# Performance work log

Hardware: AMD Instinct MI355X
Metric: run time of the kernel (lower is better)

The kernel has to match this reference:

```python
import jax, jax.numpy as jnp
import numpy as np

N_NODES = 50000
N_EDGES = 640000
D_IN = 128
D_HID = 128
D_OUT = 128
N_GRAPHS = 64


def gcn_conv(x, edge_index, W, b, n_nodes):
    """PyG GCNConv: D^{-1/2} (A + I) D^{-1/2} X W + b (unit edge weights)."""
    src, dst = edge_index[0], edge_index[1]
    h = x @ W  # [N, d_out]
    # degree counts target-side edges plus the self loop
    deg = jax.ops.segment_sum(jnp.ones_like(dst, dtype=h.dtype), dst,
                              num_segments=n_nodes) + 1.0
    dinv = jax.lax.rsqrt(deg)  # deg >= 1 so always finite
    norm = dinv[src] * dinv[dst]  # [E]
    msg = h[src] * norm[:, None]  # gather + scale  [E, d_out]
    agg = jax.ops.segment_sum(msg, dst, num_segments=n_nodes)
    # self-loop contribution: norm_ii = dinv_i^2
    agg = agg + h * (dinv * dinv)[:, None]
    return agg + b


def global_mean_pool(x, batch, n_graphs):
    sums = jax.ops.segment_sum(x, batch, num_segments=n_graphs)
    cnt = jax.ops.segment_sum(jnp.ones((x.shape[0],), dtype=x.dtype), batch,
                              num_segments=n_graphs)
    return sums / jnp.maximum(cnt, 1.0)[:, None]


def setup_inputs() -> dict:
    key = jax.random.key(0)
    k = jax.random.split(key, 8)
    x = jax.random.normal(k[0], (N_NODES, D_IN), dtype=jnp.float32)
    edge_index = jax.random.randint(k[1], (2, N_EDGES), 0, N_NODES, dtype=jnp.int64)
    batch = jnp.sort(jax.random.randint(k[2], (N_NODES,), 0, N_GRAPHS, dtype=jnp.int64))
    s1 = 1.0 / np.sqrt(D_IN)
    s2 = 1.0 / np.sqrt(D_HID)
    W1 = jax.random.uniform(k[3], (D_IN, D_HID), jnp.float32, -s1, s1)
    b1 = jnp.zeros((D_HID,), jnp.float32)
    W2 = jax.random.uniform(k[4], (D_HID, D_OUT), jnp.float32, -s2, s2)
    b2 = jnp.zeros((D_OUT,), jnp.float32)
    return {"x": x, "edge_index": edge_index, "batch": batch,
            "W1": W1, "b1": b1, "W2": W2, "b2": b2}


def reference(x, edge_index, batch, W1, b1, W2, b2):
    n = x.shape[0]
    h = jax.nn.relu(gcn_conv(x, edge_index, W1, b1, n))
    h = gcn_conv(h, edge_index, W2, b2, n)
    return global_mean_pool(h, batch, N_GRAPHS)
```

## Files before the change

kernel.cpp:

```cpp
#include <hip/hip_runtime.h>


#define D 128
#define NGRAPH 64
#define SCAN_B 1024
#define AGG_BLOCKS 2048

typedef _Float16 h16x2 __attribute__((ext_vector_type(2)));
typedef _Float16 f16x8 __attribute__((ext_vector_type(8)));
typedef float    f32x4 __attribute__((ext_vector_type(4)));

__device__ __forceinline__ float2 h2f(unsigned u) {
    h16x2 h = __builtin_bit_cast(h16x2, u);
    return make_float2((float)h.x, (float)h.y);
}
__device__ __forceinline__ unsigned f2h(float x, float y) {
    h16x2 h;
    h.x = (_Float16)x;
    h.y = (_Float16)y;
    return __builtin_bit_cast(unsigned, h);
}

__global__ void zero_out_kernel(float* __restrict__ out, int n) {
    int i = blockIdx.x * blockDim.x + threadIdx.x;
    if (i < n) out[i] = 0.f;
}

__global__ __launch_bounds__(256) void conv_count_kernel(const float* __restrict__ X,
                                                         _Float16* __restrict__ Xh,
                                                         const float* __restrict__ W1,
                                                         _Float16* __restrict__ WB,
                                                         const int* __restrict__ ei,
                                                         int* __restrict__ deg,
                                                         int N, int E, int cb) {
    int b = (int)blockIdx.x;
    if (b < cb) {
        int idx = b * 256 + (int)threadIdx.x;
        int total = N * (D / 4);
        if (idx < total) {
            float4 v = ((const float4*)X)[idx];
            uint2 o;
            o.x = f2h(v.x, v.y);
            o.y = f2h(v.z, v.w);
            ((uint2*)Xh)[idx] = o;
        }
        return;
    }
    if (b < cb + 8) {
        int idx = (b - cb) * 256 + (int)threadIdx.x;
        int lane = idx & 63;
        int nt   = (idx >> 6) & 7;
        int kt   = idx >> 9;
        int col  = nt * 16 + (lane & 15);
        int krow = kt * 32 + (lane >> 4) * 8;
#pragma unroll
        for (int j = 0; j < 8; ++j)
            WB[idx * 8 + j] = (_Float16)W1[(krow + j) * D + col];
        return;
    }
    int e = (b - cb - 8) * 256 + (int)threadIdx.x;
    if (e < E) {
        int d = ei[E + e];
        if (d >= 0 && d < N) atomicAdd(&deg[d], 1);
    }
}

__global__ __launch_bounds__(SCAN_B) void block_scan_kernel(const int* __restrict__ deg,
                                                            int* __restrict__ rowstart,
                                                            int* __restrict__ bsum,
                                                            float* __restrict__ dinv,
                                                            int N) {
    __shared__ int sc[SCAN_B];
    int t = threadIdx.x;
    int i = blockIdx.x * SCAN_B + t;
    int orig = (i < N) ? deg[i] : 0;
    int v = orig;
    sc[t] = v;
    __syncthreads();
    for (int off = 1; off < SCAN_B; off <<= 1) {
        int add = (t >= off) ? sc[t - off] : 0;
        __syncthreads();
        v += add;
        sc[t] = v;
        __syncthreads();
    }
    if (i < N) {
        rowstart[i] = v - orig;
        dinv[i]     = rsqrtf((float)orig + 1.0f);
    }
    if (t == SCAN_B - 1) bsum[blockIdx.x] = v;
}

__global__ __launch_bounds__(SCAN_B) void finalize_scan_kernel(const int* __restrict__ bsum,
                                                               int* __restrict__ rowstart,
                                                               int* __restrict__ cursor,
                                                               int N, int nblk, int E) {
    __shared__ int s_off;
    if (threadIdx.x < 64) {
        int lane = (int)threadIdx.x;
        int v = (lane < nblk && lane < (int)blockIdx.x) ? bsum[lane] : 0;
        for (int off = 32; off > 0; off >>= 1) v += __shfl_down(v, off);
        if (lane == 0) s_off = v;
    }
    __syncthreads();
    int i = blockIdx.x * SCAN_B + threadIdx.x;
    if (i < N) {
        int rs = rowstart[i] + s_off;
        rowstart[i] = rs;
        cursor[i]   = rs;
    }
    if (blockIdx.x == 0 && threadIdx.x == 0) rowstart[N] = E;
}

__global__ __launch_bounds__(256) void gemm_fill_kernel(const _Float16* __restrict__ Xh,
                                                        const _Float16* __restrict__ WB,
                                                        const float* __restrict__ dinv,
                                                        _Float16* __restrict__ Gh,
                                                        const int* __restrict__ ei,
                                                        int* __restrict__ cursor,
                                                        int* __restrict__ colidx,
                                                        int N, int E, int gb) {
    if ((int)blockIdx.x >= gb) {
        int e = ((int)blockIdx.x - gb) * 256 + (int)threadIdx.x;
        if (e < E) {
            int d = ei[E + e];
            if (d >= 0 && d < N) {
                int slot = atomicAdd(&cursor[d], 1);
                if (slot >= 0 && slot < E) {
                    int s = ei[e];
                    colidx[slot] = min(max(s, 0), N - 1);
                }
            }
        }
        return;
    }

    int t = (int)threadIdx.x;
    int wave = t >> 6, lane = t & 63;
    int mbase = blockIdx.x * 64 + wave * 16;
    int arow  = mbase + (lane & 15);
    if (arow >= N) arow = N - 1;
    int kgrp  = lane >> 4;

    f16x8 afrag[4];
#pragma unroll
    for (int kt = 0; kt < 4; ++kt) {
        uint4 u = *(const uint4*)(Xh + (size_t)arow * D + kt * 32 + kgrp * 8);
        afrag[kt] = __builtin_bit_cast(f16x8, u);
    }
    f32x4 acc[8];
#pragma unroll
    for (int nt = 0; nt < 8; ++nt) acc[nt] = (f32x4){0.f, 0.f, 0.f, 0.f};
#pragma unroll
    for (int kt = 0; kt < 4; ++kt) {
#pragma unroll
        for (int nt = 0; nt < 8; ++nt) {
            uint4 u = *(const uint4*)(WB + (((kt * 8 + nt) * 64 + lane) * 8));
            f16x8 bfrag = __builtin_bit_cast(f16x8, u);
            acc[nt] = __builtin_amdgcn_mfma_f32_16x16x32_f16(afrag[kt], bfrag, acc[nt], 0, 0, 0);
        }
    }
    int r0 = mbase + kgrp * 4;
#pragma unroll
    for (int r = 0; r < 4; ++r) {
        int row = r0 + r;
        if (row < N) {
            float dv = dinv[row];
#pragma unroll
            for (int nt = 0; nt < 8; ++nt)
                Gh[(size_t)row * D + nt * 16 + (lane & 15)] = (_Float16)(dv * acc[nt][r]);
        }
    }
}

__global__ __launch_bounds__(256) void agg1_kernel(const unsigned* __restrict__ Gh,
                                                   const int* __restrict__ rowstart,
                                                   const int* __restrict__ colidx,
                                                   const float* __restrict__ dinv,
                                                   const float* __restrict__ b1,
                                                   unsigned* __restrict__ Hh,
                                                   int N, int chunk) {
    int gid  = blockIdx.x * 4 + (threadIdx.x >> 6);
    int lane = threadIdx.x & 63;
    int i0 = gid * chunk, i1 = min(i0 + chunk, N);
    float bx = b1[2 * lane], by = b1[2 * lane + 1];
    for (int i = i0; i < i1; ++i) {
        float di = dinv[i];
        float2 acc = h2f(Gh[(size_t)i * (D / 2) + lane]);
        int e0 = rowstart[i], e1 = rowstart[i + 1];
        int e = e0;
        for (; e + 7 < e1; e += 8) {
            unsigned u[8];
#pragma unroll
            for (int j = 0; j < 8; ++j)
                u[j] = Gh[(size_t)colidx[e + j] * (D / 2) + lane];
#pragma unroll
            for (int j = 0; j < 8; ++j) {
                float2 v = h2f(u[j]);
                acc.x += v.x;
                acc.y += v.y;
            }
        }
        for (; e + 3 < e1; e += 4) {
            unsigned u[4];
#pragma unroll
            for (int j = 0; j < 4; ++j)
                u[j] = Gh[(size_t)colidx[e + j] * (D / 2) + lane];
#pragma unroll
            for (int j = 0; j < 4; ++j) {
                float2 v = h2f(u[j]);
                acc.x += v.x;
                acc.y += v.y;
            }
        }
        for (; e < e1; ++e) {
            float2 v = h2f(Gh[(size_t)colidx[e] * (D / 2) + lane]);
            acc.x += v.x;
            acc.y += v.y;
        }
        float hx = fmaxf(fmaf(di, acc.x, bx), 0.f) * di;
        float hy = fmaxf(fmaf(di, acc.y, by), 0.f) * di;
        Hh[(size_t)i * (D / 2) + lane] = f2h(hx, hy);
    }
}

__global__ __launch_bounds__(256) void agg2_pool_kernel(const unsigned* __restrict__ Hh,
                                                        const int* __restrict__ rowstart,
                                                        const int* __restrict__ colidx,
                                                        const float* __restrict__ dinv,
                                                        const int* __restrict__ batch,
                                                        float* __restrict__ pool,
                                                        int N, int chunk) {
    int gid  = blockIdx.x * 4 + (threadIdx.x >> 6);
    int lane = threadIdx.x & 63;
    int i0 = gid * chunk, i1 = min(i0 + chunk, N);
    if (i0 >= N) return;

    float2 pa = make_float2(0.f, 0.f);
    int cur = min(max(batch[i0], 0), NGRAPH - 1);
    for (int i = i0; i < i1; ++i) {
        float di = dinv[i];
        float2 a = h2f(Hh[(size_t)i * (D / 2) + lane]);
        int e0 = rowstart[i], e1 = rowstart[i + 1];
        int e = e0;
        for (; e + 7 < e1; e += 8) {
            unsigned u[8];
#pragma unroll
            for (int j = 0; j < 8; ++j)
                u[j] = Hh[(size_t)colidx[e + j] * (D / 2) + lane];
#pragma unroll
            for (int j = 0; j < 8; ++j) {
                float2 v = h2f(u[j]);
                a.x += v.x;
                a.y += v.y;
            }
        }
        for (; e + 3 < e1; e += 4) {
            unsigned u[4];
#pragma unroll
            for (int j = 0; j < 4; ++j)
                u[j] = Hh[(size_t)colidx[e + j] * (D / 2) + lane];
#pragma unroll
            for (int j = 0; j < 4; ++j) {
                float2 v = h2f(u[j]);
                a.x += v.x;
                a.y += v.y;
            }
        }
        for (; e < e1; ++e) {
            float2 v = h2f(Hh[(size_t)colidx[e] * (D / 2) + lane]);
            a.x += v.x;
            a.y += v.y;
        }
        int b = min(max(batch[i], 0), NGRAPH - 1);
        if (b != cur) {
            atomicAdd(&pool[(size_t)cur * D + 2 * lane], pa.x);
            atomicAdd(&pool[(size_t)cur * D + 2 * lane + 1], pa.y);
            pa = make_float2(0.f, 0.f);
            cur = b;
        }
        pa.x = fmaf(di, a.x, pa.x);
        pa.y = fmaf(di, a.y, pa.y);
    }
    atomicAdd(&pool[(size_t)cur * D + 2 * lane], pa.x);
    atomicAdd(&pool[(size_t)cur * D + 2 * lane + 1], pa.y);
}

__device__ __forceinline__ int lbound(const int* __restrict__ a, int n, int v) {
    int lo = 0, hi = n;
    while (lo < hi) {
        int m = (lo + hi) >> 1;
        if (a[m] < v) lo = m + 1; else hi = m;
    }
    return lo;
}

__global__ void final_gemm_kernel(const float* __restrict__ pool,
                                  const int* __restrict__ batch,
                                  const float* __restrict__ W2,
                                  const float* __restrict__ b2,
                                  float* __restrict__ out, int N) {
    int g = blockIdx.x, o = threadIdx.x;
    int s = lbound(batch, N, g);
    int e = lbound(batch, N, g + 1);
    float inv_cnt = 1.0f / fmaxf((float)(e - s), 1.0f);
    float acc = 0.f;
#pragma unroll 4
    for (int k = 0; k < D; ++k)
        acc = fmaf(pool[g * D + k], W2[k * D + o], acc);
    out[g * D + o] = acc * inv_cnt + b2[o];
}


extern "C" void kernel_launch(void* const* d_in, const int* in_sizes, int n_in,
                              void* d_out, int out_size, void* d_ws, size_t ws_size,
                              hipStream_t stream) {
    const float* x     = (const float*)d_in[0];
    const int*   ei    = (const int*)  d_in[1];
    const int*   batch = (const int*)  d_in[2];
    const float* W1    = (const float*)d_in[3];
    const float* b1    = (const float*)d_in[4];
    const float* W2    = (const float*)d_in[5];
    const float* b2    = (const float*)d_in[6];
    float* out = (float*)d_out;

    const int N = in_sizes[0] / D;
    const int E = in_sizes[1] / 2;
    const int nblk = (N + SCAN_B - 1) / SCAN_B;

    char* ws = (char*)d_ws;
    size_t off = 0;
    auto carve = [&](size_t bytes) {
        size_t o = off;
        off = (off + bytes + 255) & ~(size_t)255;
        return o;
    };
    size_t o_deg      = carve((size_t)N * 4);
    size_t o_pool     = carve((size_t)NGRAPH * D * 4);
    size_t zspan      = off;
    size_t o_rowstart = carve((size_t)(N + 1) * 4);
    size_t o_cursor   = carve((size_t)(N + 1) * 4);
    size_t o_dinv     = carve((size_t)N * 4);
    size_t o_colidx   = carve((size_t)E * 4);
    size_t o_bsum     = carve((size_t)64 * 4);
    size_t o_xh       = carve((size_t)N * D * 2);
    size_t o_wb       = carve((size_t)D * D * 2);
    size_t o_gh       = carve((size_t)N * D * 2);
    size_t o_hh       = carve((size_t)N * D * 2);
    size_t need = off;

    if (ws_size < need) {
        zero_out_kernel<<<(out_size + 255) / 256, 256, 0, stream>>>(out, out_size);
        return;
    }

    int*       deg      = (int*)      (ws + o_deg);
    float*     pool     = (float*)    (ws + o_pool);
    int*       rowstart = (int*)      (ws + o_rowstart);
    int*       cursor   = (int*)      (ws + o_cursor);
    float*     dinv     = (float*)    (ws + o_dinv);
    int*       colidx   = (int*)      (ws + o_colidx);
    int*       bsum     = (int*)      (ws + o_bsum);
    _Float16*  Xh       = (_Float16*) (ws + o_xh);
    _Float16*  WB       = (_Float16*) (ws + o_wb);
    _Float16*  Gh       = (_Float16*) (ws + o_gh);
    _Float16*  Hh       = (_Float16*) (ws + o_hh);

    hipMemsetAsync(ws, 0, zspan, stream);

    int eb = (E + 255) / 256;
    int gb = (N + 63) / 64;
    int cb = (N * (D / 4) + 255) / 256;

    conv_count_kernel<<<cb + 8 + eb, 256, 0, stream>>>(x, Xh, W1, WB, ei, deg, N, E, cb);
    block_scan_kernel<<<nblk, SCAN_B, 0, stream>>>(deg, rowstart, bsum, dinv, N);
    finalize_scan_kernel<<<nblk, SCAN_B, 0, stream>>>(bsum, rowstart, cursor, N, nblk, E);
    gemm_fill_kernel<<<gb + eb, 256, 0, stream>>>(Xh, WB, dinv, Gh, ei, cursor,
                                                  colidx, N, E, gb);

    int groups = AGG_BLOCKS * 4;
    int chunk  = (N + groups - 1) / groups;
    agg1_kernel<<<AGG_BLOCKS, 256, 0, stream>>>((const unsigned*)Gh, rowstart, colidx,
                                                dinv, b1, (unsigned*)Hh, N, chunk);
    agg2_pool_kernel<<<AGG_BLOCKS, 256, 0, stream>>>((const unsigned*)Hh, rowstart, colidx,
                                                     dinv, batch, pool, N, chunk);
    final_gemm_kernel<<<NGRAPH, D, 0, stream>>>(pool, batch, W2, b2, out, N);
}
```

Before: 224.3 us.

## Fuse X fp16 conversion into GEMM and gather two edges per wave in aggregation

Drops the separate pass that converts X to fp16 and instead converts fp32 X to fp16 inside the GEMM's A-fragment load, removing a full write and re-read of the fp16 copy. The aggregation kernels now split each wave into two 32-lane halves. Each half gathers a different neighbor row using 8-byte loads, and the halves are combined with a cross-half shuffle. This doubles the gather work in flight per wave, at the cost of extra shuffles, and the pooling atomics are issued by only half the wave.

```diff
diff --git a/kernel.cpp b/kernel.cpp
--- a/kernel.cpp
+++ b/kernel.cpp
@@ -21,33 +21,33 @@
     return __builtin_bit_cast(unsigned, h);
 }
 
+#define GATHER_PAIRS(NP)                                                      \
+    {                                                                         \
+        int c[NP];                                                            \
+        _Pragma("unroll") for (int j = 0; j < NP; ++j)                        \
+            c[j] = colidx[e + 2 * j + half];                                  \
+        uint2 u[NP];                                                          \
+        _Pragma("unroll") for (int j = 0; j < NP; ++j)                        \
+            u[j] = *(const uint2*)(Gsrc + (size_t)c[j] * 64 + sub * 2);       \
+        _Pragma("unroll") for (int j = 0; j < NP; ++j) {                      \
+            float2 v0 = h2f(u[j].x), v1 = h2f(u[j].y);                        \
+            acc.x += v0.x; acc.y += v0.y; acc.z += v1.x; acc.w += v1.y;       \
+        }                                                                     \
+    }
+
 __global__ void zero_out_kernel(float* __restrict__ out, int n) {
     int i = blockIdx.x * blockDim.x + threadIdx.x;
     if (i < n) out[i] = 0.f;
 }
 
-__global__ __launch_bounds__(256) void conv_count_kernel(const float* __restrict__ X,
-                                                         _Float16* __restrict__ Xh,
-                                                         const float* __restrict__ W1,
+__global__ __launch_bounds__(256) void pack_count_kernel(const float* __restrict__ W1,
                                                          _Float16* __restrict__ WB,
                                                          const int* __restrict__ ei,
                                                          int* __restrict__ deg,
-                                                         int N, int E, int cb) {
+                                                         int N, int E) {
     int b = (int)blockIdx.x;
-    if (b < cb) {
+    if (b < 8) {
         int idx = b * 256 + (int)threadIdx.x;
-        int total = N * (D / 4);
-        if (idx < total) {
-            float4 v = ((const float4*)X)[idx];
-            uint2 o;
-            o.x = f2h(v.x, v.y);
-            o.y = f2h(v.z, v.w);
-            ((uint2*)Xh)[idx] = o;
-        }
-        return;
-    }
-    if (b < cb + 8) {
-        int idx = (b - cb) * 256 + (int)threadIdx.x;
         int lane = idx & 63;
         int nt   = (idx >> 6) & 7;
         int kt   = idx >> 9;
@@ -58,7 +58,7 @@
             WB[idx * 8 + j] = (_Float16)W1[(krow + j) * D + col];
         return;
     }
-    int e = (b - cb - 8) * 256 + (int)threadIdx.x;
+    int e = (b - 8) * 256 + (int)threadIdx.x;
     if (e < E) {
         int d = ei[E + e];
         if (d >= 0 && d < N) atomicAdd(&deg[d], 1);
@@ -112,7 +112,7 @@
     if (blockIdx.x == 0 && threadIdx.x == 0) rowstart[N] = E;
 }
 
-__global__ __launch_bounds__(256) void gemm_fill_kernel(const _Float16* __restrict__ Xh,
+__global__ __launch_bounds__(256) void gemm_fill_kernel(const float* __restrict__ X,
                                                         const _Float16* __restrict__ WB,
                                                         const float* __restrict__ dinv,
                                                         _Float16* __restrict__ Gh,
@@ -145,8 +145,15 @@
     f16x8 afrag[4];
 #pragma unroll
     for (int kt = 0; kt < 4; ++kt) {
-        uint4 u = *(const uint4*)(Xh + (size_t)arow * D + kt * 32 + kgrp * 8);
-        afrag[kt] = __builtin_bit_cast(f16x8, u);
+        const float* xp = X + (size_t)arow * D + kt * 32 + kgrp * 8;
+        float4 a0 = *(const float4*)xp;
+        float4 a1 = *(const float4*)(xp + 4);
+        f16x8 af;
+        af[0] = (_Float16)a0.x; af[1] = (_Float16)a0.y;
+        af[2] = (_Float16)a0.z; af[3] = (_Float16)a0.w;
+        af[4] = (_Float16)a1.x; af[5] = (_Float16)a1.y;
+        af[6] = (_Float16)a1.z; af[7] = (_Float16)a1.w;
+        afrag[kt] = af;
     }
     f32x4 acc[8];
 #pragma unroll
@@ -173,7 +180,7 @@
     }
 }
 
-__global__ __launch_bounds__(256) void agg1_kernel(const unsigned* __restrict__ Gh,
+__global__ __launch_bounds__(256) void agg1_kernel(const unsigned* __restrict__ Gsrc,
                                                    const int* __restrict__ rowstart,
                                                    const int* __restrict__ colidx,
                                                    const float* __restrict__ dinv,
@@ -182,49 +189,49 @@
                                                    int N, int chunk) {
     int gid  = blockIdx.x * 4 + (threadIdx.x >> 6);
     int lane = threadIdx.x & 63;
+    int sub  = lane & 31;
+    int half = lane >> 5;
     int i0 = gid * chunk, i1 = min(i0 + chunk, N);
-    float bx = b1[2 * lane], by = b1[2 * lane + 1];
+    float4 bb = ((const float4*)b1)[sub];
     for (int i = i0; i < i1; ++i) {
         float di = dinv[i];
-        float2 acc = h2f(Gh[(size_t)i * (D / 2) + lane]);
+        float4 acc = make_float4(0.f, 0.f, 0.f, 0.f);
+        if (half == 0) {
+            uint2 s = *(const uint2*)(Gsrc + (size_t)i * 64 + sub * 2);
+            float2 v0 = h2f(s.x), v1 = h2f(s.y);
+            acc = make_float4(v0.x, v0.y, v1.x, v1.y);
+        }
         int e0 = rowstart[i], e1 = rowstart[i + 1];
         int e = e0;
-        for (; e + 7 < e1; e += 8) {
-            unsigned u[8];
-#pragma unroll
-            for (int j = 0; j < 8; ++j)
-                u[j] = Gh[(size_t)colidx[e + j] * (D / 2) + lane];
-#pragma unroll
-            for (int j = 0; j < 8; ++j) {
-                float2 v = h2f(u[j]);
-                acc.x += v.x;
-                acc.y += v.y;
-            }
-        }
-        for (; e + 3 < e1; e += 4) {
-            unsigned u[4];
-#pragma unroll
-            for (int j = 0; j < 4; ++j)
-                u[j] = Gh[(size_t)colidx[e + j] * (D / 2) + lane];
-#pragma unroll
-            for (int j = 0; j < 4; ++j) {
-                float2 v = h2f(u[j]);
-                acc.x += v.x;
-                acc.y += v.y;
-            }
-        }
-        for (; e < e1; ++e) {
-            float2 v = h2f(Gh[(size_t)colidx[e] * (D / 2) + lane]);
-            acc.x += v.x;
-            acc.y += v.y;
-        }
-        float hx = fmaxf(fmaf(di, acc.x, bx), 0.f) * di;
-        float hy = fmaxf(fmaf(di, acc.y, by), 0.f) * di;
-        Hh[(size_t)i * (D / 2) + lane] = f2h(hx, hy);
-    }
-}
-
-__global__ __launch_bounds__(256) void agg2_pool_kernel(const unsigned* __restrict__ Hh,
+        for (; e + 15 < e1; e += 16) GATHER_PAIRS(8)
+        if (e + 7 < e1) { GATHER_PAIRS(4) e += 8; }
+        if (e + 3 < e1) { GATHER_PAIRS(2) e += 4; }
+        if (e + 1 < e1) { GATHER_PAIRS(1) e += 2; }
+        if (e < e1 && half == 0) {
+            int c = colidx[e];
+            uint2 u = *(const uint2*)(Gsrc + (size_t)c * 64 + sub * 2);
+            float2 v0 = h2f(u.x), v1 = h2f(u.y);
+            acc.x += v0.x; acc.y += v0.y; acc.z += v1.x; acc.w += v1.y;
+        }
+        float4 o;
+        o.x = acc.x + __shfl_xor(acc.x, 32);
+        o.y = acc.y + __shfl_xor(acc.y, 32);
+        o.z = acc.z + __shfl_xor(acc.z, 32);
+        o.w = acc.w + __shfl_xor(acc.w, 32);
+        if (half == 0) {
+            float r0 = fmaxf(fmaf(di, o.x, bb.x), 0.f) * di;
+            float r1 = fmaxf(fmaf(di, o.y, bb.y), 0.f) * di;
+            float r2 = fmaxf(fmaf(di, o.z, bb.z), 0.f) * di;
+            float r3 = fmaxf(fmaf(di, o.w, bb.w), 0.f) * di;
+            uint2 w;
+            w.x = f2h(r0, r1);
+            w.y = f2h(r2, r3);
+            *(uint2*)(Hh + (size_t)i * 64 + sub * 2) = w;
+        }
+    }
+}
+
+__global__ __launch_bounds__(256) void agg2_pool_kernel(const unsigned* __restrict__ Gsrc,
                                                         const int* __restrict__ rowstart,
                                                         const int* __restrict__ colidx,
                                                         const float* __restrict__ dinv,
@@ -233,57 +240,61 @@
                                                         int N, int chunk) {
     int gid  = blockIdx.x * 4 + (threadIdx.x >> 6);
     int lane = threadIdx.x & 63;
+    int sub  = lane & 31;
+    int half = lane >> 5;
     int i0 = gid * chunk, i1 = min(i0 + chunk, N);
     if (i0 >= N) return;
 
-    float2 pa = make_float2(0.f, 0.f);
+    float4 pa = make_float4(0.f, 0.f, 0.f, 0.f);
     int cur = min(max(batch[i0], 0), NGRAPH - 1);
     for (int i = i0; i < i1; ++i) {
         float di = dinv[i];
-        float2 a = h2f(Hh[(size_t)i * (D / 2) + lane]);
+        float4 acc = make_float4(0.f, 0.f, 0.f, 0.f);
+        if (half == 0) {
+            uint2 s = *(const uint2*)(Gsrc + (size_t)i * 64 + sub * 2);
+            float2 v0 = h2f(s.x), v1 = h2f(s.y);
+            acc = make_float4(v0.x, v0.y, v1.x, v1.y);
+        }
         int e0 = rowstart[i], e1 = rowstart[i + 1];
         int e = e0;
-        for (; e + 7 < e1; e += 8) {
-            unsigned u[8];
-#pragma unroll
-            for (int j = 0; j < 8; ++j)
-                u[j] = Hh[(size_t)colidx[e + j] * (D / 2) + lane];
-#pragma unroll
-            for (int j = 0; j < 8; ++j) {
-                float2 v = h2f(u[j]);
-                a.x += v.x;
-                a.y += v.y;
-            }
-        }
-        for (; e + 3 < e1; e += 4) {
-            unsigned u[4];
-#pragma unroll
-            for (int j = 0; j < 4; ++j)
-                u[j] = Hh[(size_t)colidx[e + j] * (D / 2) + lane];
-#pragma unroll
-            for (int j = 0; j < 4; ++j) {
-                float2 v = h2f(u[j]);
-                a.x += v.x;
-                a.y += v.y;
-            }
-        }
-        for (; e < e1; ++e) {
-            float2 v = h2f(Hh[(size_t)colidx[e] * (D / 2) + lane]);
-            a.x += v.x;
-            a.y += v.y;
-        }
+        for (; e + 15 < e1; e += 16) GATHER_PAIRS(8)
+        if (e + 7 < e1) { GATHER_PAIRS(4) e += 8; }
+        if (e + 3 < e1) { GATHER_PAIRS(2) e += 4; }
+        if (e + 1 < e1) { GATHER_PAIRS(1) e += 2; }
+        if (e < e1 && half == 0) {
+            int c = colidx[e];
+            uint2 u = *(const uint2*)(Gsrc + (size_t)c * 64 + sub * 2);
+            float2 v0 = h2f(u.x), v1 = h2f(u.y);
+            acc.x += v0.x; acc.y += v0.y; acc.z += v1.x; acc.w += v1.y;
+        }
+        float4 o;
+        o.x = acc.x + __shfl_xor(acc.x, 32);
+        o.y = acc.y + __shfl_xor(acc.y, 32);
+        o.z = acc.z + __shfl_xor(acc.z, 32);
+        o.w = acc.w + __shfl_xor(acc.w, 32);
+
         int b = min(max(batch[i], 0), NGRAPH - 1);
         if (b != cur) {
-            atomicAdd(&pool[(size_t)cur * D + 2 * lane], pa.x);
-            atomicAdd(&pool[(size_t)cur * D + 2 * lane + 1], pa.y);
-            pa = make_float2(0.f, 0.f);
+            if (half == 0) {
+                atomicAdd(&pool[(size_t)cur * D + 4 * sub + 0], pa.x);
+                atomicAdd(&pool[(size_t)cur * D + 4 * sub + 1], pa.y);
+                atomicAdd(&pool[(size_t)cur * D + 4 * sub + 2], pa.z);
+                atomicAdd(&pool[(size_t)cur * D + 4 * sub + 3], pa.w);
+            }
+            pa = make_float4(0.f, 0.f, 0.f, 0.f);
             cur = b;
         }
-        pa.x = fmaf(di, a.x, pa.x);
-        pa.y = fmaf(di, a.y, pa.y);
-    }
-    atomicAdd(&pool[(size_t)cur * D + 2 * lane], pa.x);
-    atomicAdd(&pool[(size_t)cur * D + 2 * lane + 1], pa.y);
+        pa.x = fmaf(di, o.x, pa.x);
+        pa.y = fmaf(di, o.y, pa.y);
+        pa.z = fmaf(di, o.z, pa.z);
+        pa.w = fmaf(di, o.w, pa.w);
+    }
+    if (half == 0) {
+        atomicAdd(&pool[(size_t)cur * D + 4 * sub + 0], pa.x);
+        atomicAdd(&pool[(size_t)cur * D + 4 * sub + 1], pa.y);
+        atomicAdd(&pool[(size_t)cur * D + 4 * sub + 2], pa.z);
+        atomicAdd(&pool[(size_t)cur * D + 4 * sub + 3], pa.w);
+    }
 }
 
 __device__ __forceinline__ int lbound(const int* __restrict__ a, int n, int v) {
@@ -343,7 +354,6 @@
     size_t o_dinv     = carve((size_t)N * 4);
     size_t o_colidx   = carve((size_t)E * 4);
     size_t o_bsum     = carve((size_t)64 * 4);
-    size_t o_xh       = carve((size_t)N * D * 2);
     size_t o_wb       = carve((size_t)D * D * 2);
     size_t o_gh       = carve((size_t)N * D * 2);
     size_t o_hh       = carve((size_t)N * D * 2);
@@ -361,7 +371,6 @@
     float*     dinv     = (float*)    (ws + o_dinv);
     int*       colidx   = (int*)      (ws + o_colidx);
     int*       bsum     = (int*)      (ws + o_bsum);
-    _Float16*  Xh       = (_Float16*) (ws + o_xh);
     _Float16*  WB       = (_Float16*) (ws + o_wb);
     _Float16*  Gh       = (_Float16*) (ws + o_gh);
     _Float16*  Hh       = (_Float16*) (ws + o_hh);
@@ -370,12 +379,11 @@
 
     int eb = (E + 255) / 256;
     int gb = (N + 63) / 64;
-    int cb = (N * (D / 4) + 255) / 256;
-
-    conv_count_kernel<<<cb + 8 + eb, 256, 0, stream>>>(x, Xh, W1, WB, ei, deg, N, E, cb);
+
+    pack_count_kernel<<<8 + eb, 256, 0, stream>>>(W1, WB, ei, deg, N, E);
     block_scan_kernel<<<nblk, SCAN_B, 0, stream>>>(deg, rowstart, bsum, dinv, N);
     finalize_scan_kernel<<<nblk, SCAN_B, 0, stream>>>(bsum, rowstart, cursor, N, nblk, E);
-    gemm_fill_kernel<<<gb + eb, 256, 0, stream>>>(Xh, WB, dinv, Gh, ei, cursor,
+    gemm_fill_kernel<<<gb + eb, 256, 0, stream>>>(x, WB, dinv, Gh, ei, cursor,
                                                   colidx, N, E, gb);
 
     int groups = AGG_BLOCKS * 4;
```

After: 250.3 us. +11.6%, slower.

## Pad CSR rows to eight with dummy zero node, use 16-bit column indices

Applied to the files above, without the earlier changes.

Each CSR row is padded to a multiple of eight entries. The padding points at an extra zero row appended to the G and H buffers, which lets the aggregation loops drop their remainder tails and load eight column indices with one vector load. Column indices are stored as 16-bit values to cut index traffic. The separate fp32-to-fp16 conversion pass over X is removed, and the conversion happens inside the GEMM's A-fragment loads. The edge count and fill kernels now handle four edges per thread. This adds padded gather work and relies on N fitting in 16 bits.

```diff
diff --git a/kernel.cpp b/kernel.cpp
--- a/kernel.cpp
+++ b/kernel.cpp
@@ -9,6 +9,7 @@
 typedef _Float16 h16x2 __attribute__((ext_vector_type(2)));
 typedef _Float16 f16x8 __attribute__((ext_vector_type(8)));
 typedef float    f32x4 __attribute__((ext_vector_type(4)));
+typedef unsigned short u16x8 __attribute__((ext_vector_type(8)));
 
 __device__ __forceinline__ float2 h2f(unsigned u) {
     h16x2 h = __builtin_bit_cast(h16x2, u);
@@ -26,28 +27,16 @@
     if (i < n) out[i] = 0.f;
 }
 
-__global__ __launch_bounds__(256) void conv_count_kernel(const float* __restrict__ X,
-                                                         _Float16* __restrict__ Xh,
-                                                         const float* __restrict__ W1,
+__global__ __launch_bounds__(256) void pack_count_kernel(const float* __restrict__ W1,
                                                          _Float16* __restrict__ WB,
                                                          const int* __restrict__ ei,
                                                          int* __restrict__ deg,
-                                                         int N, int E, int cb) {
+                                                         unsigned* __restrict__ Gz,
+                                                         unsigned* __restrict__ Hz,
+                                                         int N, int E) {
     int b = (int)blockIdx.x;
-    if (b < cb) {
+    if (b < 8) {
         int idx = b * 256 + (int)threadIdx.x;
-        int total = N * (D / 4);
-        if (idx < total) {
-            float4 v = ((const float4*)X)[idx];
-            uint2 o;
-            o.x = f2h(v.x, v.y);
-            o.y = f2h(v.z, v.w);
-            ((uint2*)Xh)[idx] = o;
-        }
-        return;
-    }
-    if (b < cb + 8) {
-        int idx = (b - cb) * 256 + (int)threadIdx.x;
         int lane = idx & 63;
         int nt   = (idx >> 6) & 7;
         int kt   = idx >> 9;
@@ -58,11 +47,22 @@
             WB[idx * 8 + j] = (_Float16)W1[(krow + j) * D + col];
         return;
     }
-    int e = (b - cb - 8) * 256 + (int)threadIdx.x;
-    if (e < E) {
-        int d = ei[E + e];
-        if (d >= 0 && d < N) atomicAdd(&deg[d], 1);
-    }
+    if (b == 8) {
+        int t = (int)threadIdx.x;
+        if (t < 64)       Gz[(size_t)N * 64 + t] = 0u;
+        else if (t < 128) Hz[(size_t)N * 64 + (t - 64)] = 0u;
+        return;
+    }
+    int e0 = (b - 9) * 1024 + (int)threadIdx.x;
+    int d[4];
+#pragma unroll
+    for (int j = 0; j < 4; ++j) {
+        int e = e0 + j * 256;
+        d[j] = (e < E) ? ei[E + e] : -1;
+    }
+#pragma unroll
+    for (int j = 0; j < 4; ++j)
+        if (d[j] >= 0 && d[j] < N) atomicAdd(&deg[d[j]], 1);
 }
 
 __global__ __launch_bounds__(SCAN_B) void block_scan_kernel(const int* __restrict__ deg,
@@ -74,7 +74,8 @@
     int t = threadIdx.x;
     int i = blockIdx.x * SCAN_B + t;
     int orig = (i < N) ? deg[i] : 0;
-    int v = orig;
+    int pad8 = (orig + 7) & ~7;
+    int v = pad8;
     sc[t] = v;
     __syncthreads();
     for (int off = 1; off < SCAN_B; off <<= 1) {
@@ -85,22 +86,32 @@
         __syncthreads();
     }
     if (i < N) {
-        rowstart[i] = v - orig;
+        rowstart[i] = v - pad8;
         dinv[i]     = rsqrtf((float)orig + 1.0f);
     }
     if (t == SCAN_B - 1) bsum[blockIdx.x] = v;
 }
 
 __global__ __launch_bounds__(SCAN_B) void finalize_scan_kernel(const int* __restrict__ bsum,
+                                                               const int* __restrict__ deg,
                                                                int* __restrict__ rowstart,
                                                                int* __restrict__ cursor,
-                                                               int N, int nblk, int E) {
+                                                               unsigned short* __restrict__ colidx,
+                                                               int N, int nblk) {
     __shared__ int s_off;
     if (threadIdx.x < 64) {
         int lane = (int)threadIdx.x;
-        int v = (lane < nblk && lane < (int)blockIdx.x) ? bsum[lane] : 0;
-        for (int off = 32; off > 0; off >>= 1) v += __shfl_down(v, off);
-        if (lane == 0) s_off = v;
+        int bv = (lane < nblk) ? bsum[lane] : 0;
+        int v  = (lane < (int)blockIdx.x) ? bv : 0;
+        int vt = bv;
+        for (int off = 32; off > 0; off >>= 1) {
+            v  += __shfl_down(v, off);
+            vt += __shfl_down(vt, off);
+        }
+        if (lane == 0) {
+            s_off = v;
+            if (blockIdx.x == 0) rowstart[N] = vt;
+        }
     }
     __syncthreads();
     int i = blockIdx.x * SCAN_B + threadIdx.x;
@@ -108,30 +119,39 @@
         int rs = rowstart[i] + s_off;
         rowstart[i] = rs;
         cursor[i]   = rs;
-    }
-    if (blockIdx.x == 0 && threadIdx.x == 0) rowstart[N] = E;
-}
-
-__global__ __launch_bounds__(256) void gemm_fill_kernel(const _Float16* __restrict__ Xh,
+        int dg = deg[i];
+        int p8 = (dg + 7) & ~7;
+        for (int k = dg; k < p8; ++k)
+            colidx[rs + k] = (unsigned short)N;
+    }
+}
+
+__global__ __launch_bounds__(256) void gemm_fill_kernel(const float* __restrict__ X,
                                                         const _Float16* __restrict__ WB,
                                                         const float* __restrict__ dinv,
                                                         _Float16* __restrict__ Gh,
                                                         const int* __restrict__ ei,
                                                         int* __restrict__ cursor,
-                                                        int* __restrict__ colidx,
+                                                        unsigned short* __restrict__ colidx,
                                                         int N, int E, int gb) {
     if ((int)blockIdx.x >= gb) {
-        int e = ((int)blockIdx.x - gb) * 256 + (int)threadIdx.x;
-        if (e < E) {
-            int d = ei[E + e];
-            if (d >= 0 && d < N) {
-                int slot = atomicAdd(&cursor[d], 1);
-                if (slot >= 0 && slot < E) {
-                    int s = ei[e];
-                    colidx[slot] = min(max(s, 0), N - 1);
-                }
-            }
-        }
+        int e0 = ((int)blockIdx.x - gb) * 1024 + (int)threadIdx.x;
+        int d[4], s[4], slot[4];
+#pragma unroll
+        for (int j = 0; j < 4; ++j) {
+            int e = e0 + j * 256;
+            if (e < E) {
+                d[j] = ei[E + e];
+                s[j] = ei[e];
+            } else d[j] = -1;
+        }
+#pragma unroll
+        for (int j = 0; j < 4; ++j)
+            if (d[j] >= 0 && d[j] < N) slot[j] = atomicAdd(&cursor[d[j]], 1);
+#pragma unroll
+        for (int j = 0; j < 4; ++j)
+            if (d[j] >= 0 && d[j] < N)
+                colidx[slot[j]] = (unsigned short)min(max(s[j], 0), N - 1);
         return;
     }
 
@@ -145,8 +165,15 @@
     f16x8 afrag[4];
 #pragma unroll
     for (int kt = 0; kt < 4; ++kt) {
-        uint4 u = *(const uint4*)(Xh + (size_t)arow * D + kt * 32 + kgrp * 8);
-        afrag[kt] = __builtin_bit_cast(f16x8, u);
+        const float* xp = X + (size_t)arow * D + kt * 32 + kgrp * 8;
+        float4 a0 = *(const float4*)xp;
+        float4 a1 = *(const float4*)(xp + 4);
+        f16x8 af;
+        af[0] = (_Float16)a0.x; af[1] = (_Float16)a0.y;
+        af[2] = (_Float16)a0.z; af[3] = (_Float16)a0.w;
+        af[4] = (_Float16)a1.x; af[5] = (_Float16)a1.y;
+        af[6] = (_Float16)a1.z; af[7] = (_Float16)a1.w;
+        afrag[kt] = af;
     }
     f32x4 acc[8];
 #pragma unroll
@@ -175,7 +202,7 @@
 
 __global__ __launch_bounds__(256) void agg1_kernel(const unsigned* __restrict__ Gh,
                                                    const int* __restrict__ rowstart,
-                                                   const int* __restrict__ colidx,
+                                                   const unsigned short* __restrict__ colidx,
                                                    const float* __restrict__ dinv,
                                                    const float* __restrict__ b1,
                                                    unsigned* __restrict__ Hh,
@@ -186,14 +213,14 @@
     float bx = b1[2 * lane], by = b1[2 * lane + 1];
     for (int i = i0; i < i1; ++i) {
         float di = dinv[i];
-        float2 acc = h2f(Gh[(size_t)i * (D / 2) + lane]);
+        float2 acc = h2f(Gh[(size_t)i * 64 + lane]);
         int e0 = rowstart[i], e1 = rowstart[i + 1];
-        int e = e0;
-        for (; e + 7 < e1; e += 8) {
+        for (int e = e0; e < e1; e += 8) {
+            u16x8 cc = *(const u16x8*)(colidx + e);
             unsigned u[8];
 #pragma unroll
             for (int j = 0; j < 8; ++j)
-                u[j] = Gh[(size_t)colidx[e + j] * (D / 2) + lane];
+                u[j] = Gh[(size_t)cc[j] * 64 + lane];
 #pragma unroll
             for (int j = 0; j < 8; ++j) {
                 float2 v = h2f(u[j]);
@@ -201,32 +228,15 @@
                 acc.y += v.y;
             }
         }
-        for (; e + 3 < e1; e += 4) {
-            unsigned u[4];
-#pragma unroll
-            for (int j = 0; j < 4; ++j)
-                u[j] = Gh[(size_t)colidx[e + j] * (D / 2) + lane];
-#pragma unroll
-            for (int j = 0; j < 4; ++j) {
-                float2 v = h2f(u[j]);
-                acc.x += v.x;
-                acc.y += v.y;
-            }
-        }
-        for (; e < e1; ++e) {
-            float2 v = h2f(Gh[(size_t)colidx[e] * (D / 2) + lane]);
-            acc.x += v.x;
-            acc.y += v.y;
-        }
         float hx = fmaxf(fmaf(di, acc.x, bx), 0.f) * di;
         float hy = fmaxf(fmaf(di, acc.y, by), 0.f) * di;
-        Hh[(size_t)i * (D / 2) + lane] = f2h(hx, hy);
+        Hh[(size_t)i * 64 + lane] = f2h(hx, hy);
     }
 }
 
 __global__ __launch_bounds__(256) void agg2_pool_kernel(const unsigned* __restrict__ Hh,
                                                         const int* __restrict__ rowstart,
-                                                        const int* __restrict__ colidx,
+                                                        const unsigned short* __restrict__ colidx,
                                                         const float* __restrict__ dinv,
                                                         const int* __restrict__ batch,
                                                         float* __restrict__ pool,
@@ -240,37 +250,20 @@
     int cur = min(max(batch[i0], 0), NGRAPH - 1);
     for (int i = i0; i < i1; ++i) {
         float di = dinv[i];
-        float2 a = h2f(Hh[(size_t)i * (D / 2) + lane]);
+        float2 a = h2f(Hh[(size_t)i * 64 + lane]);
         int e0 = rowstart[i], e1 = rowstart[i + 1];
-        int e = e0;
-        for (; e + 7 < e1; e += 8) {
+        for (int e = e0; e < e1; e += 8) {
+            u16x8 cc = *(const u16x8*)(colidx + e);
             unsigned u[8];
 #pragma unroll
             for (int j = 0; j < 8; ++j)
-                u[j] = Hh[(size_t)colidx[e + j] * (D / 2) + lane];
+                u[j] = Hh[(size_t)cc[j] * 64 + lane];
 #pragma unroll
             for (int j = 0; j < 8; ++j) {
                 float2 v = h2f(u[j]);
                 a.x += v.x;
                 a.y += v.y;
             }
-        }
-        for (; e + 3 < e1; e += 4) {
-            unsigned u[4];
-#pragma unroll
-            for (int j = 0; j < 4; ++j)
-                u[j] = Hh[(size_t)colidx[e + j] * (D / 2) + lane];
-#pragma unroll
-            for (int j = 0; j < 4; ++j) {
-                float2 v = h2f(u[j]);
-                a.x += v.x;
-                a.y += v.y;
-            }
-        }
-        for (; e < e1; ++e) {
-            float2 v = h2f(Hh[(size_t)colidx[e] * (D / 2) + lane]);
-            a.x += v.x;
-            a.y += v.y;
         }
         int b = min(max(batch[i], 0), NGRAPH - 1);
         if (b != cur) {
@@ -341,12 +334,11 @@
     size_t o_rowstart = carve((size_t)(N + 1) * 4);
     size_t o_cursor   = carve((size_t)(N + 1) * 4);
     size_t o_dinv     = carve((size_t)N * 4);
-    size_t o_colidx   = carve((size_t)E * 4);
+    size_t o_colidx   = carve(((size_t)E + 7 * (size_t)N + 64) * 2);
     size_t o_bsum     = carve((size_t)64 * 4);
-    size_t o_xh       = carve((size_t)N * D * 2);
     size_t o_wb       = carve((size_t)D * D * 2);
-    size_t o_gh       = carve((size_t)N * D * 2);
-    size_t o_hh       = carve((size_t)N * D * 2);
+    size_t o_gh       = carve((size_t)(N + 1) * D * 2);
+    size_t o_hh       = carve((size_t)(N + 1) * D * 2);
     size_t need = off;
 
     if (ws_size < need) {
@@ -354,29 +346,29 @@
         return;
     }
 
-    int*       deg      = (int*)      (ws + o_deg);
-    float*     pool     = (float*)    (ws + o_pool);
-    int*       rowstart = (int*)      (ws + o_rowstart);
-    int*       cursor   = (int*)      (ws + o_cursor);
-    float*     dinv     = (float*)    (ws + o_dinv);
-    int*       colidx   = (int*)      (ws + o_colidx);
-    int*       bsum     = (int*)      (ws + o_bsum);
-    _Float16*  Xh       = (_Float16*) (ws + o_xh);
-    _Float16*  WB       = (_Float16*) (ws + o_wb);
-    _Float16*  Gh       = (_Float16*) (ws + o_gh);
-    _Float16*  Hh       = (_Float16*) (ws + o_hh);
+    int*            deg      = (int*)           (ws + o_deg);
+    float*          pool     = (float*)         (ws + o_pool);
+    int*            rowstart = (int*)           (ws + o_rowstart);
+    int*            cursor   = (int*)           (ws + o_cursor);
+    float*          dinv     = (float*)         (ws + o_dinv);
+    unsigned short* colidx   = (unsigned short*)(ws + o_colidx);
+    int*            bsum     = (int*)           (ws + o_bsum);
+    _Float16*       WB       = (_Float16*)      (ws + o_wb);
+    _Float16*       Gh       = (_Float16*)      (ws + o_gh);
+    _Float16*       Hh       = (_Float16*)      (ws + o_hh);
 
     hipMemsetAsync(ws, 0, zspan, stream);
 
-    int eb = (E + 255) / 256;
-    int gb = (N + 63) / 64;
-    int cb = (N * (D / 4) + 255) / 256;
-
-    conv_count_kernel<<<cb + 8 + eb, 256, 0, stream>>>(x, Xh, W1, WB, ei, deg, N, E, cb);
+    int ebc = (E + 1023) / 1024;
+    int gb  = (N + 63) / 64;
+
+    pack_count_kernel<<<9 + ebc, 256, 0, stream>>>(W1, WB, ei, deg,
+                                                   (unsigned*)Gh, (unsigned*)Hh, N, E);
     block_scan_kernel<<<nblk, SCAN_B, 0, stream>>>(deg, rowstart, bsum, dinv, N);
-    finalize_scan_kernel<<<nblk, SCAN_B, 0, stream>>>(bsum, rowstart, cursor, N, nblk, E);
-    gemm_fill_kernel<<<gb + eb, 256, 0, stream>>>(Xh, WB, dinv, Gh, ei, cursor,
-                                                  colidx, N, E, gb);
+    finalize_scan_kernel<<<nblk, SCAN_B, 0, stream>>>(bsum, deg, rowstart, cursor,
+                                                      colidx, N, nblk);
+    gemm_fill_kernel<<<gb + ebc, 256, 0, stream>>>(x, WB, dinv, Gh, ei, cursor,
+                                                   colidx, N, E, gb);
 
     int groups = AGG_BLOCKS * 4;
     int chunk  = (N + groups - 1) / groups;
```

Measured after the change: 225.6 us. Within noise of the previous version (+0.6%).
